# Optimization experiments

Hardware: AMD Instinct MI355X
Metric: run time of the kernel (lower is better)

## Reference

```python
import jax, jax.numpy as jnp
import numpy as np

D_MODEL = 128
N_LAYERS = 2
D_STATE = 16
D_CONV = 4
EXPAND = 2
GRID = 16
D_INNER = D_MODEL * EXPAND
DT_RANK = (D_MODEL + 15) // 16  # mamba_ssm default: ceil(d_model/16) = 8
BATCH = 128
SEQ = 200


def setup_inputs() -> dict:
    key = jax.random.key(0)
    ks = jax.random.split(key, 24)
    L = N_LAYERS

    def rn(k, shape, scale=0.02):
        return jax.random.normal(k, shape, dtype=jnp.float32) * scale

    A_init = jnp.log(jnp.broadcast_to(
        jnp.arange(1, D_STATE + 1, dtype=jnp.float32), (L, D_INNER, D_STATE)))
    kan_scale = 1.0 / (np.sqrt(D_MODEL) * np.sqrt(GRID))
    return {
        "x": jax.random.normal(ks[0], (BATCH, SEQ, D_MODEL), dtype=jnp.float32),
        "in_w": rn(ks[1], (L, 2 * D_INNER, D_MODEL)),
        "out_w": rn(ks[2], (L, D_MODEL, D_INNER)),
        "conv_w_f": rn(ks[3], (L, D_INNER, D_CONV), 0.1),
        "conv_b_f": rn(ks[4], (L, D_INNER), 0.01),
        "conv_w_b": rn(ks[5], (L, D_INNER, D_CONV), 0.1),
        "conv_b_b": rn(ks[6], (L, D_INNER), 0.01),
        "xproj_w_f": rn(ks[7], (L, DT_RANK + 2 * D_STATE, D_INNER)),
        "xproj_w_b": rn(ks[8], (L, DT_RANK + 2 * D_STATE, D_INNER)),
        "dtproj_w_f": rn(ks[9], (L, D_INNER, DT_RANK), 0.1),
        "dtproj_b_f": rn(ks[10], (L, D_INNER), 0.01),
        "dtproj_w_b": rn(ks[11], (L, D_INNER, DT_RANK), 0.1),
        "dtproj_b_b": rn(ks[12], (L, D_INNER), 0.01),
        "A_log_f": A_init,
        "A_log_b": A_init,
        "D_f": jnp.ones((L, D_INNER), jnp.float32),
        "D_b": jnp.ones((L, D_INNER), jnp.float32),
        "ln1_w": jnp.ones((L, D_MODEL), jnp.float32),
        "ln1_b": jnp.zeros((L, D_MODEL), jnp.float32),
        "ln_w": jnp.ones((L, D_MODEL), jnp.float32),
        "ln_b": jnp.zeros((L, D_MODEL), jnp.float32),
        "kan_coef": jax.random.normal(ks[13], (L, 2, D_MODEL, D_MODEL, GRID), dtype=jnp.float32) * kan_scale,
    }


def _ln(x, w, b, eps=1e-12):
    u = x.mean(-1, keepdims=True)
    s = ((x - u) ** 2).mean(-1, keepdims=True)
    return w * (x - u) / jnp.sqrt(s + eps) + b


def _silu(x):
    return x * jax.nn.sigmoid(x)


def _mamba(x, in_w, out_w, conv_w, conv_b, xp_w, dt_w, dt_b, A_log, Dp):
    # x: (B, L, d_model). Faithful to mamba_ssm Mamba (bias=False proj, conv_bias=True).
    B, L, _ = x.shape
    xz = jnp.einsum('bld,ed->ble', x, in_w)          # (B, L, 2*d_inner)
    xi, z = jnp.split(xz, 2, axis=-1)
    # causal depthwise conv over L
    xp = jnp.pad(xi, ((0, 0), (D_CONV - 1, 0), (0, 0)))
    xc = sum(xp[:, k:k + L, :] * conv_w[:, k] for k in range(D_CONV)) + conv_b
    xc = _silu(xc)                                    # (B, L, d_inner)
    dbl = jnp.einsum('ble,fe->blf', xc, xp_w)         # (B, L, dt_rank+2*d_state)
    dt = jax.nn.softplus(
        jnp.einsum('blr,dr->bld', dbl[..., :DT_RANK], dt_w) + dt_b)
    Bm = dbl[..., DT_RANK:DT_RANK + D_STATE]          # (B, L, d_state)
    Cm = dbl[..., DT_RANK + D_STATE:]
    A = -jnp.exp(A_log)                               # (d_inner, d_state)

    def step(h, inp):
        dt_t, u_t, b_t, c_t = inp                     # (B,di),(B,di),(B,ds),(B,ds)
        h = jnp.exp(dt_t[:, :, None] * A) * h + (dt_t * u_t)[:, :, None] * b_t[:, None, :]
        return h, jnp.einsum('bds,bs->bd', h, c_t)

    h0 = jnp.zeros((B, D_INNER, D_STATE), x.dtype)
    _, ys = jax.lax.scan(step, h0, (jnp.moveaxis(dt, 1, 0), jnp.moveaxis(xc, 1, 0),
                                    jnp.moveaxis(Bm, 1, 0), jnp.moveaxis(Cm, 1, 0)))
    y = jnp.moveaxis(ys, 0, 1) + xc * Dp              # (B, L, d_inner)
    y = y * _silu(z)
    return jnp.einsum('ble,de->bld', y, out_w)


def _kan(x, coef):
    # coef: (2, outdim, inputdim, grid)
    shp = x.shape
    xf = x.reshape(-1, shp[-1])                       # (N, d)
    kk = jnp.arange(1, GRID + 1, dtype=x.dtype)
    ang = xf[:, :, None] * kk                         # (N, d, grid)
    y = (jnp.einsum('nig,jig->nj', jnp.cos(ang), coef[0])
         + jnp.einsum('nig,jig->nj', jnp.sin(ang), coef[1]))
    return y.reshape(shp[:-1] + (coef.shape[1],))


def reference(x, in_w, out_w, conv_w_f, conv_b_f, conv_w_b, conv_b_b,
              xproj_w_f, xproj_w_b, dtproj_w_f, dtproj_b_f, dtproj_w_b, dtproj_b_b,
              A_log_f, A_log_b, D_f, D_b, ln1_w, ln1_b, ln_w, ln_b, kan_coef):
    feats = []
    h = x
    for l in range(N_LAYERS):
        o = _ln(h, ln1_w[l], ln1_b[l])
        f = _mamba(o, in_w[l], out_w[l], conv_w_f[l], conv_b_f[l],
                   xproj_w_f[l], dtproj_w_f[l], dtproj_b_f[l], A_log_f[l], D_f[l])
        b = _mamba(o[:, ::-1], in_w[l], out_w[l], conv_w_b[l], conv_b_b[l],
                   xproj_w_b[l], dtproj_w_b[l], dtproj_b_b[l], A_log_b[l], D_b[l])[:, ::-1]
        o = _ln(f + b, ln_w[l], ln_b[l])
        o = _kan(o, kan_coef[l])  # dropout p=0.0 (eval) -> identity
        h = o + h
        feats.append(h)
    return sum(feats) / len(feats)
```

## Files before the change

### kernel.cpp

```cpp
#include <hip/hip_runtime.h>
#include <hip/hip_bf16.h>
#include <cmath>

#define BATCH 128
#define SEQ 200
#define DMODEL 128
#define DINNER 256
#define DSTATE 16
#define NTOK (BATCH * SEQ)

typedef __bf16 bf16x8 __attribute__((ext_vector_type(8)));
typedef float f32x4 __attribute__((ext_vector_type(4)));

__device__ __forceinline__ unsigned short f2bf(float f) {
  union { float f; unsigned u; } x{f};
  const unsigned r = x.u + 0x7fffu + ((x.u >> 16) & 1u);
  return (unsigned short)(r >> 16);
}
__device__ __forceinline__ float bf2f(unsigned short h) {
  union { unsigned u; float f; } x{(unsigned)h << 16};
  return x.f;
}
__device__ __forceinline__ void split2(float a, float b, unsigned& hp, unsigned& lp) {
  const unsigned short ha = f2bf(a), hb = f2bf(b);
  const float ra = a - bf2f(ha), rb = b - bf2f(hb);
  hp = (unsigned)ha | ((unsigned)hb << 16);
  lp = (unsigned)f2bf(ra) | ((unsigned)f2bf(rb) << 16);
}

template <int CTRL>
__device__ __forceinline__ float dpp_add(float v) {
  const int r = __builtin_amdgcn_update_dpp(0, __float_as_int(v), CTRL, 0xF, 0xF, true);
  return v + __int_as_float(r);
}

__device__ __forceinline__ float silu_f(float x) {
  return x / (1.f + __expf(-x));
}

__global__ __launch_bounds__(256) void ln_kernel(const float* __restrict__ in,
                                                 const float* __restrict__ w,
                                                 const float* __restrict__ b,
                                                 float* __restrict__ out) {
  const int wv = threadIdx.x >> 6;
  const int lane = threadIdx.x & 63;
  const int row = blockIdx.x * 4 + wv;
  const float2 v = *(const float2*)(in + (size_t)row * DMODEL + lane * 2);
  float s = v.x + v.y;
#pragma unroll
  for (int o = 32; o; o >>= 1) s += __shfl_xor(s, o, 64);
  const float u = s * (1.f / 128.f);
  const float dx = v.x - u, dy = v.y - u;
  float sq = dx * dx + dy * dy;
#pragma unroll
  for (int o = 32; o; o >>= 1) sq += __shfl_xor(sq, o, 64);
  const float inv = rsqrtf(sq * (1.f / 128.f) + 1e-12f);
  const float2 wv2 = *(const float2*)(w + lane * 2);
  const float2 bv2 = *(const float2*)(b + lane * 2);
  float2 o2v;
  o2v.x = fmaf(wv2.x, dx * inv, bv2.x);
  o2v.y = fmaf(wv2.y, dy * inv, bv2.y);
  *(float2*)(out + (size_t)row * DMODEL + lane * 2) = o2v;
}

__global__ __launch_bounds__(256) void wprep(const float* __restrict__ in_w,
                                             const float* __restrict__ xpwf,
                                             const float* __restrict__ xpwb,
                                             const float* __restrict__ out_w,
                                             unsigned short* __restrict__ iwH,
                                             unsigned short* __restrict__ iwL,
                                             unsigned short* __restrict__ xfH,
                                             unsigned short* __restrict__ xfL,
                                             unsigned short* __restrict__ xbH,
                                             unsigned short* __restrict__ xbL,
                                             unsigned short* __restrict__ owH,
                                             unsigned short* __restrict__ owL) {
  const int idx = blockIdx.x * 256 + threadIdx.x;
  float w;
  unsigned short *H, *L;
  int off;
  if (idx < 65536)      { w = in_w[idx];        H = iwH; L = iwL; off = idx; }
  else if (idx < 75776) { w = xpwf[idx - 65536]; H = xfH; L = xfL; off = idx - 65536; }
  else if (idx < 86016) { w = xpwb[idx - 75776]; H = xbH; L = xbL; off = idx - 75776; }
  else                  { w = out_w[idx - 86016]; H = owH; L = owL; off = idx - 86016; }
  const unsigned short h = f2bf(w);
  H[off] = h;
  L[off] = f2bf(w - bf2f(h));
}

template <int MODE>
__global__ __launch_bounds__(256) void gemm_c(const float* __restrict__ A1,
                                              const float* __restrict__ A2,
                                              const unsigned short* __restrict__ Whi,
                                              const unsigned short* __restrict__ Wlo,
                                              float* __restrict__ C,
                                              const unsigned short* __restrict__ Whi2,
                                              const unsigned short* __restrict__ Wlo2,
                                              float* __restrict__ C2,
                                              int M, int N, int K) {
  __shared__ unsigned short AshH[64 * 40], AshL[64 * 40];
  __shared__ unsigned short BshH[128 * 40], BshL[128 * 40];
  const float* Ause = A1;
  const unsigned short* WH = Whi;
  const unsigned short* WL = Wlo;
  float* Cuse = C;
  if (MODE == 2 && blockIdx.z == 1) { Ause = A2; WH = Whi2; WL = Wlo2; Cuse = C2; }
  const int tid = threadIdx.x;
  const int m0 = blockIdx.y * 64;
  const int n0 = blockIdx.x * 128;
  const int lane = tid & 63;
  const int wid = tid >> 6;
  const int arow = lane & 15;
  const int kch = (lane >> 4) * 8;
  const int bcol = wid * 32 + (lane & 15);
  f32x4 acc[4][2] = {};
  for (int k0 = 0; k0 < K; k0 += 32) {
    __syncthreads();
    {
      const int row = tid >> 2;
      const int koff = (tid & 3) * 8;
      const int m = m0 + row;
      float4 v0 = *(const float4*)(Ause + (size_t)m * K + k0 + koff);
      float4 v1 = *(const float4*)(Ause + (size_t)m * K + k0 + koff + 4);
      unsigned h0, l0, h1, l1, h2, l2, h3, l3;
      split2(v0.x, v0.y, h0, l0);
      split2(v0.z, v0.w, h1, l1);
      split2(v1.x, v1.y, h2, l2);
      split2(v1.z, v1.w, h3, l3);
      *(uint4*)&AshH[row * 40 + koff] = make_uint4(h0, h1, h2, h3);
      *(uint4*)&AshL[row * 40 + koff] = make_uint4(l0, l1, l2, l3);
    }
    {
      const int row = tid >> 1;
      const int koff = (tid & 1) * 16;
      const int n = n0 + row;
      uint4 wh0 = make_uint4(0, 0, 0, 0), wh1 = wh0, wl0 = wh0, wl1 = wh0;
      if (n < N) {
        wh0 = *(const uint4*)(WH + (size_t)n * K + k0 + koff);
        wh1 = *(const uint4*)(WH + (size_t)n * K + k0 + koff + 8);
        wl0 = *(const uint4*)(WL + (size_t)n * K + k0 + koff);
        wl1 = *(const uint4*)(WL + (size_t)n * K + k0 + koff + 8);
      }
      *(uint4*)&BshH[row * 40 + koff] = wh0;
      *(uint4*)&BshH[row * 40 + koff + 8] = wh1;
      *(uint4*)&BshL[row * 40 + koff] = wl0;
      *(uint4*)&BshL[row * 40 + koff + 8] = wl1;
    }
    __syncthreads();
    const bf16x8 bh0 = *(const bf16x8*)&BshH[bcol * 40 + kch];
    const bf16x8 bh1 = *(const bf16x8*)&BshH[(bcol + 16) * 40 + kch];
    const bf16x8 bl0 = *(const bf16x8*)&BshL[bcol * 40 + kch];
    const bf16x8 bl1 = *(const bf16x8*)&BshL[(bcol + 16) * 40 + kch];
#pragma unroll
    for (int g = 0; g < 4; ++g) {
      const bf16x8 ah = *(const bf16x8*)&AshH[(g * 16 + arow) * 40 + kch];
      const bf16x8 al = *(const bf16x8*)&AshL[(g * 16 + arow) * 40 + kch];
      acc[g][0] = __builtin_amdgcn_mfma_f32_16x16x32_bf16(ah, bh0, acc[g][0], 0, 0, 0);
      acc[g][0] = __builtin_amdgcn_mfma_f32_16x16x32_bf16(al, bh0, acc[g][0], 0, 0, 0);
      acc[g][0] = __builtin_amdgcn_mfma_f32_16x16x32_bf16(ah, bl0, acc[g][0], 0, 0, 0);
      acc[g][1] = __builtin_amdgcn_mfma_f32_16x16x32_bf16(ah, bh1, acc[g][1], 0, 0, 0);
      acc[g][1] = __builtin_amdgcn_mfma_f32_16x16x32_bf16(al, bh1, acc[g][1], 0, 0, 0);
      acc[g][1] = __builtin_amdgcn_mfma_f32_16x16x32_bf16(ah, bl1, acc[g][1], 0, 0, 0);
    }
  }
  const int q0 = (lane >> 4) * 4;
#pragma unroll
  for (int g = 0; g < 4; ++g)
#pragma unroll
    for (int fc = 0; fc < 2; ++fc)
#pragma unroll
      for (int q = 0; q < 4; ++q) {
        const int m = m0 + g * 16 + q0 + q;
        const int n = n0 + wid * 32 + fc * 16 + (lane & 15);
        if (n < N) Cuse[(size_t)m * N + n] = acc[g][fc][q];
      }
}

__global__ __launch_bounds__(256) void gemm_oln(const float* __restrict__ A1,
                                                const float* __restrict__ A2v,
                                                const float* __restrict__ Zp,
                                                const unsigned short* __restrict__ Whi,
                                                const unsigned short* __restrict__ Wlo,
                                                const float* __restrict__ lw,
                                                const float* __restrict__ lb,
                                                float* __restrict__ o2out) {
  __shared__ unsigned short AshH[64 * 40], AshL[64 * 40];
  __shared__ unsigned short BshH[128 * 40], BshL[128 * 40];
  __shared__ float Csh[64][132];
  const int tid = threadIdx.x;
  const int m0 = blockIdx.x * 64;
  const int lane = tid & 63;
  const int wid = tid >> 6;
  const int arow = lane & 15;
  const int kch = (lane >> 4) * 8;
  const int bcol = wid * 32 + (lane & 15);
  f32x4 acc[4][2] = {};
  for (int k0 = 0; k0 < 256; k0 += 32) {
    __syncthreads();
    {
      const int row = tid >> 2;
      const int koff = (tid & 3) * 8;
      const int m = m0 + row;
      float4 v0 = *(const float4*)(A1 + (size_t)m * 256 + k0 + koff);
      float4 v1 = *(const float4*)(A1 + (size_t)m * 256 + k0 + koff + 4);
      const float4 u0 = *(const float4*)(A2v + (size_t)m * 256 + k0 + koff);
      const float4 u1 = *(const float4*)(A2v + (size_t)m * 256 + k0 + koff + 4);
      const float4 z0 = *(const float4*)(Zp + (size_t)m * 512 + k0 + koff);
      const float4 z1 = *(const float4*)(Zp + (size_t)m * 512 + k0 + koff + 4);
      v0.x = (v0.x + u0.x) * silu_f(z0.x);
      v0.y = (v0.y + u0.y) * silu_f(z0.y);
      v0.z = (v0.z + u0.z) * silu_f(z0.z);
      v0.w = (v0.w + u0.w) * silu_f(z0.w);
      v1.x = (v1.x + u1.x) * silu_f(z1.x);
      v1.y = (v1.y + u1.y) * silu_f(z1.y);
      v1.z = (v1.z + u1.z) * silu_f(z1.z);
      v1.w = (v1.w + u1.w) * silu_f(z1.w);
      unsigned h0, l0, h1, l1, h2, l2, h3, l3;
      split2(v0.x, v0.y, h0, l0);
      split2(v0.z, v0.w, h1, l1);
      split2(v1.x, v1.y, h2, l2);
      split2(v1.z, v1.w, h3, l3);
      *(uint4*)&AshH[row * 40 + koff] = make_uint4(h0, h1, h2, h3);
      *(uint4*)&AshL[row * 40 + koff] = make_uint4(l0, l1, l2, l3);
    }
    {
      const int row = tid >> 1;
      const int koff = (tid & 1) * 16;
      const uint4 wh0 = *(const uint4*)(Whi + (size_t)row * 256 + k0 + koff);
      const uint4 wh1 = *(const uint4*)(Whi + (size_t)row * 256 + k0 + koff + 8);
      const uint4 wl0 = *(const uint4*)(Wlo + (size_t)row * 256 + k0 + koff);
      const uint4 wl1 = *(const uint4*)(Wlo + (size_t)row * 256 + k0 + koff + 8);
      *(uint4*)&BshH[row * 40 + koff] = wh0;
      *(uint4*)&BshH[row * 40 + koff + 8] = wh1;
      *(uint4*)&BshL[row * 40 + koff] = wl0;
      *(uint4*)&BshL[row * 40 + koff + 8] = wl1;
    }
    __syncthreads();
    const bf16x8 bh0 = *(const bf16x8*)&BshH[bcol * 40 + kch];
    const bf16x8 bh1 = *(const bf16x8*)&BshH[(bcol + 16) * 40 + kch];
    const bf16x8 bl0 = *(const bf16x8*)&BshL[bcol * 40 + kch];
    const bf16x8 bl1 = *(const bf16x8*)&BshL[(bcol + 16) * 40 + kch];
#pragma unroll
    for (int g = 0; g < 4; ++g) {
      const bf16x8 ah = *(const bf16x8*)&AshH[(g * 16 + arow) * 40 + kch];
      const bf16x8 al = *(const bf16x8*)&AshL[(g * 16 + arow) * 40 + kch];
      acc[g][0] = __builtin_amdgcn_mfma_f32_16x16x32_bf16(ah, bh0, acc[g][0], 0, 0, 0);
      acc[g][0] = __builtin_amdgcn_mfma_f32_16x16x32_bf16(al, bh0, acc[g][0], 0, 0, 0);
      acc[g][0] = __builtin_amdgcn_mfma_f32_16x16x32_bf16(ah, bl0, acc[g][0], 0, 0, 0);
      acc[g][1] = __builtin_amdgcn_mfma_f32_16x16x32_bf16(ah, bh1, acc[g][1], 0, 0, 0);
      acc[g][1] = __builtin_amdgcn_mfma_f32_16x16x32_bf16(al, bh1, acc[g][1], 0, 0, 0);
      acc[g][1] = __builtin_amdgcn_mfma_f32_16x16x32_bf16(ah, bl1, acc[g][1], 0, 0, 0);
    }
  }
  __syncthreads();
  const int q0 = (lane >> 4) * 4;
#pragma unroll
  for (int g = 0; g < 4; ++g)
#pragma unroll
    for (int fc = 0; fc < 2; ++fc)
#pragma unroll
      for (int q = 0; q < 4; ++q)
        Csh[g * 16 + q0 + q][wid * 32 + fc * 16 + (lane & 15)] = acc[g][fc][q];
  __syncthreads();
  const int row = tid >> 2;
  const int c0 = (tid & 3) * 32;
  float vloc[32];
  float s = 0.f;
#pragma unroll
  for (int j = 0; j < 32; ++j) {
    vloc[j] = Csh[row][c0 + j];
    s += vloc[j];
  }
  s = dpp_add<0xB1>(s);
  s = dpp_add<0x4E>(s);
  const float u = s * (1.f / 128.f);
  float sq = 0.f;
#pragma unroll
  for (int j = 0; j < 32; ++j) {
    const float dd = vloc[j] - u;
    sq += dd * dd;
  }
  sq = dpp_add<0xB1>(sq);
  sq = dpp_add<0x4E>(sq);
  const float inv = rsqrtf(sq * (1.f / 128.f) + 1e-12f);
  float* outp = o2out + (size_t)(m0 + row) * 128 + c0;
#pragma unroll
  for (int j4 = 0; j4 < 8; ++j4) {
    const float4 wv = *(const float4*)(lw + c0 + j4 * 4);
    const float4 bv = *(const float4*)(lb + c0 + j4 * 4);
    float4 o;
    o.x = fmaf(wv.x, (vloc[j4 * 4 + 0] - u) * inv, bv.x);
    o.y = fmaf(wv.y, (vloc[j4 * 4 + 1] - u) * inv, bv.y);
    o.z = fmaf(wv.z, (vloc[j4 * 4 + 2] - u) * inv, bv.z);
    o.w = fmaf(wv.w, (vloc[j4 * 4 + 3] - u) * inv, bv.w);
    *(float4*)(outp + j4 * 4) = o;
  }
}

__global__ __launch_bounds__(256) void conv_silu_kernel(const float* __restrict__ xz,
                                                        const float* __restrict__ cwf,
                                                        const float* __restrict__ cbf,
                                                        const float* __restrict__ cwb,
                                                        const float* __restrict__ cbb,
                                                        float* __restrict__ xcf,
                                                        float* __restrict__ xcb) {
  const int n0 = blockIdx.x * 8;
  const int l0 = n0 % SEQ;
  const int e = threadIdx.x;
  const float4 wf = *(const float4*)(cwf + e * 4);
  const float4 wb = *(const float4*)(cwb + e * 4);
  const float bfv = cbf[e], bbv = cbb[e];
  const float* px = xz + (size_t)n0 * 512 + e;
  float w[7];
#pragma unroll
  for (int j = 0; j < 6; ++j) {
    const int l = l0 - 3 + j;
    w[j] = (l >= 0 && l < SEQ) ? px[(j - 3) * 512] : 0.f;
  }
#pragma unroll
  for (int t = 0; t < 8; ++t) {
    const int l = l0 + t;
    w[6] = (l + 3 < SEQ) ? px[(t + 3) * 512] : 0.f;
    const float af = fmaf(wf.x, w[0], fmaf(wf.y, w[1], fmaf(wf.z, w[2], fmaf(wf.w, w[3], bfv))));
    const float ab = fmaf(wb.x, w[6], fmaf(wb.y, w[5], fmaf(wb.z, w[4], fmaf(wb.w, w[3], bbv))));
    xcf[(size_t)(n0 + t) * DINNER + e] = silu_f(af);
    xcb[(size_t)(n0 + t) * DINNER + e] = silu_f(ab);
#pragma unroll
    for (int j = 0; j < 6; ++j) w[j] = w[j + 1];
  }
}

__global__ __launch_bounds__(256) void dtsp_kernel2(const float* __restrict__ dblF,
                                                    const float* __restrict__ dblB,
                                                    const float* __restrict__ dtwF,
                                                    const float* __restrict__ dtbF,
                                                    const float* __restrict__ dtwB,
                                                    const float* __restrict__ dtbB,
                                                    float* __restrict__ dtF,
                                                    float* __restrict__ dtB) {
  const int bwd = blockIdx.y;
  const float* __restrict__ dbl = bwd ? dblB : dblF;
  const float* __restrict__ dtw = bwd ? dtwB : dtwF;
  const float* __restrict__ dtb = bwd ? dtbB : dtbF;
  float* __restrict__ dt = bwd ? dtB : dtF;
  __shared__ float r[8][8];
  const int n0 = blockIdx.x * 8;
  const int d = threadIdx.x;
  if (threadIdx.x < 64) {
    const int tt = threadIdx.x >> 3, j = threadIdx.x & 7;
    r[tt][j] = dbl[(size_t)(n0 + tt) * 40 + j];
  }
  const float4 w0 = *(const float4*)(dtw + d * 8);
  const float4 w1 = *(const float4*)(dtw + d * 8 + 4);
  const float bd = dtb[d];
  __syncthreads();
#pragma unroll
  for (int tt = 0; tt < 8; ++tt) {
    float acc = bd;
    acc += r[tt][0] * w0.x + r[tt][1] * w0.y + r[tt][2] * w0.z + r[tt][3] * w0.w;
    acc += r[tt][4] * w1.x + r[tt][5] * w1.y + r[tt][6] * w1.z + r[tt][7] * w1.w;
    const float sp = acc > 20.f ? acc : log1pf(__expf(acc));
    dt[(size_t)(n0 + tt) * DINNER + d] = sp;
  }
}

template <int SX, int SB>
__device__ __forceinline__ void scan_body(const float* __restrict__ dt,
                                          float* __restrict__ xc,
                                          const float* __restrict__ dbl,
                                          const float* __restrict__ Alog,
                                          const float* __restrict__ Dp,
                                          int bb) {
  const int lane = threadIdx.x & 63;
  const int wid = threadIdx.x >> 6;
  const int q = lane & 3;
  const int dl = lane >> 2;
  const int d = blockIdx.x * 64 + wid * 16 + dl;
  const float LOG2E = 1.44269504f;
  const float4 al = *(const float4*)(Alog + d * DSTATE + q * 4);
  const float4 A2 = make_float4(-__expf(al.x) * LOG2E, -__expf(al.y) * LOG2E,
                                -__expf(al.z) * LOG2E, -__expf(al.w) * LOG2E);
  const float Dd = Dp[d];
  const int t0 = (SX > 0) ? 0 : (SEQ - 1);
  int offX = (bb * SEQ + t0) * DINNER + d;
  int offB = (bb * SEQ + t0) * 40 + 8 + q * 4;
  float4 h = make_float4(0.f, 0.f, 0.f, 0.f);

  float adt[4], au[4]; float4 aB[4], aC[4];
  float bdt[4], bu[4]; float4 bB[4], bC[4];

  auto loadg = [&](float* gdt, float* gu, float4* gB, float4* gC, int oX, int oB) {
#pragma unroll
    for (int k = 0; k < 4; ++k) {
      gdt[k] = dt[oX + k * SX];
      gu[k] = xc[oX + k * SX];
      gB[k] = *(const float4*)(dbl + oB + k * SB);
      gC[k] = *(const float4*)(dbl + oB + k * SB + 16);
    }
  };
  auto computeg = [&](const float* gdt, const float* gu, const float4* gB,
                      const float4* gC, int oX) {
#pragma unroll
    for (int k = 0; k < 4; ++k) {
      const float dtv = gdt[k];
      const float u = gu[k];
      const float du = dtv * u;
      float4 a;
      a.x = exp2f(dtv * A2.x);
      a.y = exp2f(dtv * A2.y);
      a.z = exp2f(dtv * A2.z);
      a.w = exp2f(dtv * A2.w);
      h.x = fmaf(a.x, h.x, du * gB[k].x);
      h.y = fmaf(a.y, h.y, du * gB[k].y);
      h.z = fmaf(a.z, h.z, du * gB[k].z);
      h.w = fmaf(a.w, h.w, du * gB[k].w);
      float pp = fmaf(h.w, gC[k].w, fmaf(h.z, gC[k].z, fmaf(h.y, gC[k].y, h.x * gC[k].x)));
      pp = dpp_add<0xB1>(pp);
      pp = dpp_add<0x4E>(pp);
      if (q == 0) xc[oX + k * SX] = fmaf(u, Dd, pp);
    }
  };

  loadg(adt, au, aB, aC, offX, offB);
  for (int t = 0; t < SEQ; t += 8) {
    loadg(bdt, bu, bB, bC, offX + 4 * SX, offB + 4 * SB);
    computeg(adt, au, aB, aC, offX);
    if (t + 8 < SEQ) loadg(adt, au, aB, aC, offX + 8 * SX, offB + 8 * SB);
    computeg(bdt, bu, bB, bC, offX + 4 * SX);
    offX += 8 * SX;
    offB += 8 * SB;
  }
}

__global__ __launch_bounds__(256, 4) void scan_kernel5(
    const float* __restrict__ dtF, float* xcF, const float* __restrict__ dblF,
    const float* __restrict__ AlogF, const float* __restrict__ DF,
    const float* __restrict__ dtB, float* xcB, const float* __restrict__ dblB,
    const float* __restrict__ AlogB, const float* __restrict__ DB) {
  if (blockIdx.z == 0)
    scan_body<DINNER, 40>(dtF, xcF, dblF, AlogF, DF, blockIdx.y);
  else
    scan_body<-DINNER, -40>(dtB, xcB, dblB, AlogB, DB, blockIdx.y);
}

__global__ __launch_bounds__(256) void kan_prep(const float* __restrict__ coef,
                                                unsigned short* __restrict__ Wt) {
  const int idx = blockIdx.x * 256 + threadIdx.x;
  const int k = idx & 31;
  const int j = (idx >> 5) & 127;
  const int i = idx >> 12;
  const int c = k >> 4, g = k & 15;
  Wt[idx] = f2bf(coef[(((size_t)c * 128 + j) * 128 + i) * 16 + g]);
}

__global__ __launch_bounds__(256) void kan_mfma(const float* __restrict__ x,
                                                const unsigned short* __restrict__ Wt,
                                                const float* __restrict__ hin,
                                                float* __restrict__ hout,
                                                float* __restrict__ accum,
                                                int first) {
  __shared__ float Xs[128 * 64];
  __shared__ unsigned short F[2][64 * 40];
  __shared__ unsigned short Wsh[2][128 * 40];
  const int tid = threadIdx.x;
  const int n0 = blockIdx.x * 64;
  const int wid = tid >> 6;
  const int lane = tid & 63;
  {
    const int tok = tid & 63;
    const int cq = tid >> 6;
#pragma unroll
    for (int r = 0; r < 8; ++r) {
      const int i0 = cq * 32 + r * 4;
      const float4 v = *(const float4*)(x + (size_t)(n0 + tok) * 128 + i0);
      Xs[(i0 + 0) * 64 + tok] = v.x;
      Xs[(i0 + 1) * 64 + tok] = v.y;
      Xs[(i0 + 2) * 64 + tok] = v.z;
      Xs[(i0 + 3) * 64 + tok] = v.w;
    }
  }
  const int fs = tid >> 7;
  const int fn = (tid & 127) >> 1;
  const int fh = tid & 1;
  const int wrow = tid & 127;
  const int arow = lane & 15;
  const int kch = (lane >> 4) * 8;
  const int bcol = wid * 32 + (lane & 15);
  f32x4 acc[4][2] = {};
  for (int ii = 0; ii < 128; ii += 2) {
    __syncthreads();
    {
      const uint4* src = (const uint4*)(Wt + (size_t)(ii + fs) * 4096 + wrow * 32);
      uint4* dst = (uint4*)&Wsh[fs][wrow * 40];
      dst[0] = src[0]; dst[1] = src[1]; dst[2] = src[2]; dst[3] = src[3];
    }
    {
      const float xv = Xs[(ii + fs) * 64 + fn];
      const float c1 = __cosf(xv), s1 = __sinf(xv);
      float c, s;
      if (fh == 0) { c = c1; s = s1; }
      else {
        const float y = xv * 9.f;
        c = __cosf(y); s = __sinf(y);
      }
      unsigned int* Fu = (unsigned int*)F[fs];
#pragma unroll
      for (int p = 0; p < 4; ++p) {
        const float c2 = c * c1 - s * s1;
        const float s2 = s * c1 + c * s1;
        Fu[fn * 20 + fh * 4 + p]     = (unsigned)f2bf(c) | ((unsigned)f2bf(c2) << 16);
        Fu[fn * 20 + 8 + fh * 4 + p] = (unsigned)f2bf(s) | ((unsigned)f2bf(s2) << 16);
        c = c2 * c1 - s2 * s1;
        s = s2 * c1 + c2 * s1;
      }
    }
    __syncthreads();
#pragma unroll
    for (int sl = 0; sl < 2; ++sl) {
      const bf16x8 b0 = *(const bf16x8*)&Wsh[sl][bcol * 40 + kch];
      const bf16x8 b1 = *(const bf16x8*)&Wsh[sl][(bcol + 16) * 40 + kch];
#pragma unroll
      for (int g = 0; g < 4; ++g) {
        const bf16x8 a = *(const bf16x8*)&F[sl][(g * 16 + arow) * 40 + kch];
        acc[g][0] = __builtin_amdgcn_mfma_f32_16x16x32_bf16(a, b0, acc[g][0], 0, 0, 0);
        acc[g][1] = __builtin_amdgcn_mfma_f32_16x16x32_bf16(a, b1, acc[g][1], 0, 0, 0);
      }
    }
  }
  const int q0 = (lane >> 4) * 4;
#pragma unroll
  for (int g = 0; g < 4; ++g)
#pragma unroll
    for (int fc = 0; fc < 2; ++fc)
#pragma unroll
      for (int q = 0; q < 4; ++q) {
        const int n = n0 + g * 16 + q0 + q;
        const int j = wid * 32 + fc * 16 + (lane & 15);
        const size_t off = (size_t)n * 128 + j;
        const float v = acc[g][fc][q] + hin[off];
        hout[off] = v;
        const float a = 0.5f * v;
        accum[off] = first ? a : (accum[off] + a);
      }
}

extern "C" void kernel_launch(void* const* d_in, const int* in_sizes, int n_in,
                              void* d_out, int out_size, void* d_ws, size_t ws_size,
                              hipStream_t stream) {
  (void)in_sizes; (void)n_in; (void)out_size;
  const float* x     = (const float*)d_in[0];
  const float* in_w  = (const float*)d_in[1];
  const float* out_w = (const float*)d_in[2];
  const float* cwf   = (const float*)d_in[3];
  const float* cbf   = (const float*)d_in[4];
  const float* cwb   = (const float*)d_in[5];
  const float* cbb   = (const float*)d_in[6];
  const float* xpwf  = (const float*)d_in[7];
  const float* xpwb  = (const float*)d_in[8];
  const float* dtwf  = (const float*)d_in[9];
  const float* dtbf  = (const float*)d_in[10];
  const float* dtwb  = (const float*)d_in[11];
  const float* dtbb  = (const float*)d_in[12];
  const float* Alogf = (const float*)d_in[13];
  const float* Alogb = (const float*)d_in[14];
  const float* Dfp   = (const float*)d_in[15];
  const float* Dbp   = (const float*)d_in[16];
  const float* ln1w  = (const float*)d_in[17];
  const float* ln1b  = (const float*)d_in[18];
  const float* lnw   = (const float*)d_in[19];
  const float* lnb   = (const float*)d_in[20];
  const float* kanc  = (const float*)d_in[21];
  float* outp = (float*)d_out;

  int C = 128;
  while (C > 8) {
    const size_t need = ((size_t)761856 + (size_t)2000 * C * SEQ) * 4;
    if (need <= ws_size) break;
    C >>= 1;
  }
  const int T = C * SEQ;

  unsigned short* usbase = (unsigned short*)d_ws;
  unsigned short* Wt_l[2];
  unsigned short *iwH[2], *iwL[2], *xfH[2], *xfL[2], *xbH[2], *xbL[2], *owH[2], *owL[2];
  for (int l = 0; l < 2; ++l) {
    Wt_l[l] = usbase + (size_t)l * 524288;
    unsigned short* q = usbase + 2 * 524288 + (size_t)l * 237568;
    iwH[l] = q;           iwL[l] = q + 65536;
    xfH[l] = q + 131072;  xfL[l] = q + 141312;
    xbH[l] = q + 151552;  xbL[l] = q + 161792;
    owH[l] = q + 172032;  owL[l] = q + 204800;
  }
  float* pf = (float*)d_ws + 761856;
  float* o1   = pf; pf += (size_t)T * 128;
  float* xzb  = pf; pf += (size_t)T * 512;
  float* xcf  = pf; pf += (size_t)T * 256;
  float* xcb  = pf; pf += (size_t)T * 256;
  float* dblf = pf; pf += (size_t)T * 40;
  float* dblb = pf; pf += (size_t)T * 40;
  float* dtf  = pf; pf += (size_t)T * 256;
  float* dtb  = pf; pf += (size_t)T * 256;
  float* o2   = pf; pf += (size_t)T * 128;
  float* hbuf = pf; pf += (size_t)T * 128;

  for (int l = 0; l < 2; ++l) {
    wprep<<<464, 256, 0, stream>>>(in_w + (size_t)l * 65536, xpwf + (size_t)l * 10240,
                                   xpwb + (size_t)l * 10240, out_w + (size_t)l * 32768,
                                   iwH[l], iwL[l], xfH[l], xfL[l],
                                   xbH[l], xbL[l], owH[l], owL[l]);
    kan_prep<<<2048, 256, 0, stream>>>(kanc + (size_t)l * 2 * 128 * 128 * 16, Wt_l[l]);
  }

  for (int b0 = 0; b0 < BATCH; b0 += C) {
    const size_t tok0 = (size_t)b0 * SEQ;
    for (int l = 0; l < 2; ++l) {
      const float* hin = (l == 0) ? (x + tok0 * 128) : hbuf;
      ln_kernel<<<T / 4, 256, 0, stream>>>(hin, ln1w + l * 128, ln1b + l * 128, o1);
      gemm_c<0><<<dim3(4, T / 64), 256, 0, stream>>>(
          o1, (const float*)nullptr, iwH[l], iwL[l], xzb,
          (const unsigned short*)nullptr, (const unsigned short*)nullptr,
          (float*)nullptr, T, 512, 128);
      conv_silu_kernel<<<T / 8, 256, 0, stream>>>(xzb, cwf + l * 1024, cbf + l * 256,
                                                  cwb + l * 1024, cbb + l * 256, xcf, xcb);
      gemm_c<2><<<dim3(1, T / 64, 2), 256, 0, stream>>>(
          xcf, xcb, xfH[l], xfL[l], dblf, xbH[l], xbL[l], dblb, T, 40, 256);
      dtsp_kernel2<<<dim3(T / 8, 2), 256, 0, stream>>>(dblf, dblb,
                                                       dtwf + l * 2048, dtbf + l * 256,
                                                       dtwb + l * 2048, dtbb + l * 256,
                                                       dtf, dtb);
      scan_kernel5<<<dim3(4, C, 2), 256, 0, stream>>>(
          dtf, xcf, dblf, Alogf + l * 4096, Dfp + l * 256,
          dtb, xcb, dblb, Alogb + l * 4096, Dbp + l * 256);
      gemm_oln<<<T / 64, 256, 0, stream>>>(xcf, xcb, xzb + 256, owH[l], owL[l],
                                           lnw + l * 128, lnb + l * 128, o2);
      kan_mfma<<<T / 64, 256, 0, stream>>>(o2, Wt_l[l], hin, hbuf,
                                           outp + tok0 * 128, l == 0 ? 1 : 0);
    }
  }
}
```

Baseline: 621.3 us.

## Triple-buffer scan loads and double-buffer KAN GEMM with swizzled LDS

```diff
diff --git a/kernel.cpp b/kernel.cpp
--- a/kernel.cpp
+++ b/kernel.cpp
@@ -388,6 +388,7 @@
 
   float adt[4], au[4]; float4 aB[4], aC[4];
   float bdt[4], bu[4]; float4 bB[4], bC[4];
+  float cdt[4], cu[4]; float4 cB[4], cC[4];
 
   auto loadg = [&](float* gdt, float* gu, float4* gB, float4* gC, int oX, int oB) {
 #pragma unroll
@@ -422,17 +423,22 @@
   };
 
   loadg(adt, au, aB, aC, offX, offB);
-  for (int t = 0; t < SEQ; t += 8) {
-    loadg(bdt, bu, bB, bC, offX + 4 * SX, offB + 4 * SB);
+  loadg(bdt, bu, bB, bC, offX + 4 * SX, offB + 4 * SB);
+  for (int t = 0; t < 192; t += 12) {
+    loadg(cdt, cu, cB, cC, offX + 8 * SX, offB + 8 * SB);
     computeg(adt, au, aB, aC, offX);
-    if (t + 8 < SEQ) loadg(adt, au, aB, aC, offX + 8 * SX, offB + 8 * SB);
+    loadg(adt, au, aB, aC, offX + 12 * SX, offB + 12 * SB);
     computeg(bdt, bu, bB, bC, offX + 4 * SX);
-    offX += 8 * SX;
-    offB += 8 * SB;
-  }
-}
-
-__global__ __launch_bounds__(256, 4) void scan_kernel5(
+    loadg(bdt, bu, bB, bC, offX + 16 * SX, offB + 16 * SB);
+    computeg(cdt, cu, cB, cC, offX + 8 * SX);
+    offX += 12 * SX;
+    offB += 12 * SB;
+  }
+  computeg(adt, au, aB, aC, offX);
+  computeg(bdt, bu, bB, bC, offX + 4 * SX);
+}
+
+__global__ __launch_bounds__(256, 4) void scan_kernel6(
     const float* __restrict__ dtF, float* xcF, const float* __restrict__ dblF,
     const float* __restrict__ AlogF, const float* __restrict__ DF,
     const float* __restrict__ dtB, float* xcB, const float* __restrict__ dblB,
@@ -459,73 +465,85 @@
                                                 float* __restrict__ hout,
                                                 float* __restrict__ accum,
                                                 int first) {
-  __shared__ float Xs[128 * 64];
-  __shared__ unsigned short F[2][64 * 40];
-  __shared__ unsigned short Wsh[2][128 * 40];
+  __shared__ unsigned short F[2][2][64 * 40];
+  __shared__ unsigned short Wsh[2][2][128 * 40];
   const int tid = threadIdx.x;
   const int n0 = blockIdx.x * 64;
   const int wid = tid >> 6;
   const int lane = tid & 63;
-  {
-    const int tok = tid & 63;
-    const int cq = tid >> 6;
-#pragma unroll
-    for (int r = 0; r < 8; ++r) {
-      const int i0 = cq * 32 + r * 4;
-      const float4 v = *(const float4*)(x + (size_t)(n0 + tok) * 128 + i0);
-      Xs[(i0 + 0) * 64 + tok] = v.x;
-      Xs[(i0 + 1) * 64 + tok] = v.y;
-      Xs[(i0 + 2) * 64 + tok] = v.z;
-      Xs[(i0 + 3) * 64 + tok] = v.w;
-    }
-  }
   const int fs = tid >> 7;
   const int fn = (tid & 127) >> 1;
   const int fh = tid & 1;
   const int wrow = tid & 127;
+  const int wx = (wrow >> 3) & 3;
+  const int fx = (fn >> 3) & 3;
   const int arow = lane & 15;
-  const int kch = (lane >> 4) * 8;
+  const int kc = lane >> 4;
   const int bcol = wid * 32 + (lane & 15);
+  const float* xrow = x + (size_t)(n0 + fn) * 128 + fs;
+  const unsigned short* wsrc0 = Wt + (size_t)fs * 4096 + (size_t)wrow * 32;
+
+  uint4 wr0, wr1, wr2, wr3;
+  float xv;
+  auto stageW = [&](int buf) {
+    unsigned short* wdst = &Wsh[buf][fs][wrow * 40];
+    *(uint4*)(wdst + (0 ^ wx) * 8) = wr0;
+    *(uint4*)(wdst + (1 ^ wx) * 8) = wr1;
+    *(uint4*)(wdst + (2 ^ wx) * 8) = wr2;
+    *(uint4*)(wdst + (3 ^ wx) * 8) = wr3;
+  };
+  auto features = [&](int buf) {
+    const float c1 = __cosf(xv), s1 = __sinf(xv);
+    float c, s;
+    if (fh == 0) { c = c1; s = s1; }
+    else { const float y = xv * 9.f; c = __cosf(y); s = __sinf(y); }
+    unsigned* Fu = (unsigned*)&F[buf][fs][fn * 40];
+#pragma unroll
+    for (int p = 0; p < 4; ++p) {
+      const float c2 = c * c1 - s * s1;
+      const float s2 = s * c1 + c * s1;
+      Fu[((fh ^ fx) << 2) | p]         = (unsigned)f2bf(c) | ((unsigned)f2bf(c2) << 16);
+      Fu[(((2 + fh) ^ fx) << 2) | p]   = (unsigned)f2bf(s) | ((unsigned)f2bf(s2) << 16);
+      c = c2 * c1 - s2 * s1;
+      s = s2 * c1 + c2 * s1;
+    }
+  };
+
   f32x4 acc[4][2] = {};
-  for (int ii = 0; ii < 128; ii += 2) {
-    __syncthreads();
-    {
-      const uint4* src = (const uint4*)(Wt + (size_t)(ii + fs) * 4096 + wrow * 32);
-      uint4* dst = (uint4*)&Wsh[fs][wrow * 40];
-      dst[0] = src[0]; dst[1] = src[1]; dst[2] = src[2]; dst[3] = src[3];
-    }
-    {
-      const float xv = Xs[(ii + fs) * 64 + fn];
-      const float c1 = __cosf(xv), s1 = __sinf(xv);
-      float c, s;
-      if (fh == 0) { c = c1; s = s1; }
-      else {
-        const float y = xv * 9.f;
-        c = __cosf(y); s = __sinf(y);
-      }
-      unsigned int* Fu = (unsigned int*)F[fs];
-#pragma unroll
-      for (int p = 0; p < 4; ++p) {
-        const float c2 = c * c1 - s * s1;
-        const float s2 = s * c1 + c * s1;
-        Fu[fn * 20 + fh * 4 + p]     = (unsigned)f2bf(c) | ((unsigned)f2bf(c2) << 16);
-        Fu[fn * 20 + 8 + fh * 4 + p] = (unsigned)f2bf(s) | ((unsigned)f2bf(s2) << 16);
-        c = c2 * c1 - s2 * s1;
-        s = s2 * c1 + c2 * s1;
-      }
-    }
-    __syncthreads();
+  {
+    const uint4* src = (const uint4*)wsrc0;
+    wr0 = src[0]; wr1 = src[1]; wr2 = src[2]; wr3 = src[3];
+    xv = xrow[0];
+    stageW(0);
+    features(0);
+  }
+  __syncthreads();
+  for (int r = 0; r < 64; ++r) {
+    const int cur = r & 1;
+    if (r < 63) {
+      const uint4* src = (const uint4*)(wsrc0 + (size_t)(2 * (r + 1)) * 4096);
+      wr0 = src[0]; wr1 = src[1]; wr2 = src[2]; wr3 = src[3];
+      xv = xrow[2 * (r + 1)];
+    }
 #pragma unroll
     for (int sl = 0; sl < 2; ++sl) {
-      const bf16x8 b0 = *(const bf16x8*)&Wsh[sl][bcol * 40 + kch];
-      const bf16x8 b1 = *(const bf16x8*)&Wsh[sl][(bcol + 16) * 40 + kch];
+      const int bx0 = (bcol >> 3) & 3;
+      const int bx1 = ((bcol + 16) >> 3) & 3;
+      const bf16x8 b0 = *(const bf16x8*)&Wsh[cur][sl][bcol * 40 + (kc ^ bx0) * 8];
+      const bf16x8 b1 = *(const bf16x8*)&Wsh[cur][sl][(bcol + 16) * 40 + (kc ^ bx1) * 8];
 #pragma unroll
       for (int g = 0; g < 4; ++g) {
-        const bf16x8 a = *(const bf16x8*)&F[sl][(g * 16 + arow) * 40 + kch];
+        const int ar = g * 16 + arow;
+        const bf16x8 a = *(const bf16x8*)&F[cur][sl][ar * 40 + (kc ^ ((ar >> 3) & 3)) * 8];
         acc[g][0] = __builtin_amdgcn_mfma_f32_16x16x32_bf16(a, b0, acc[g][0], 0, 0, 0);
         acc[g][1] = __builtin_amdgcn_mfma_f32_16x16x32_bf16(a, b1, acc[g][1], 0, 0, 0);
       }
     }
+    if (r < 63) {
+      stageW(cur ^ 1);
+      features(cur ^ 1);
+    }
+    __syncthreads();
   }
   const int q0 = (lane >> 4) * 4;
 #pragma unroll
@@ -628,7 +646,7 @@
                                                        dtwf + l * 2048, dtbf + l * 256,
                                                        dtwb + l * 2048, dtbb + l * 256,
                                                        dtf, dtb);
-      scan_kernel5<<<dim3(4, C, 2), 256, 0, stream>>>(
+      scan_kernel6<<<dim3(4, C, 2), 256, 0, stream>>>(
           dtf, xcf, dblf, Alogf + l * 4096, Dfp + l * 256,
           dtb, xcb, dblb, Alogb + l * 4096, Dbp + l * 256);
       gemm_oln<<<T / 64, 256, 0, stream>>>(xcf, xcb, xzb + 256, owH[l], owL[l],
```

Result: slower. 891.0 us (+43.4%).
